# Kernel optimization log

Measured on AMD Instinct MI355X. Metric: run time of the kernel, lower is better.

Reference implementation:

```python
import jax, jax.numpy as jnp
import numpy as np

N_EMBD = 1024
N_HEAD = 16
LN_EPS = 1e-5

def setup_inputs() -> dict:
    key = jax.random.key(0)
    ks = jax.random.split(key, 12)
    B, T, C = 2, 2048, N_EMBD
    s = lambda k, shape, scale=0.02: (jax.random.normal(k, shape, dtype=jnp.float32) * scale)
    return {
        "x": jax.random.normal(ks[0], (B, T, C), dtype=jnp.float32),
        "ln1_g": jnp.ones((C,), jnp.float32),
        "ln1_b": jnp.zeros((C,), jnp.float32),
        "W_attn": s(ks[1], (C, 3 * C)),
        "b_attn": jnp.zeros((3 * C,), jnp.float32),
        "W_o": s(ks[2], (C, C)),
        "b_o": jnp.zeros((C,), jnp.float32),
        "ln2_g": jnp.ones((C,), jnp.float32),
        "ln2_b": jnp.zeros((C,), jnp.float32),
        "W_fc": s(ks[3], (C, 4 * C)),
        "b_fc": jnp.zeros((4 * C,), jnp.float32),
        "W_fc2": s(ks[4], (4 * C, C)),
        "b_fc2": jnp.zeros((C,), jnp.float32),
    }

def _layernorm(x, g, b):
    mu = jnp.mean(x, axis=-1, keepdims=True)
    var = jnp.mean(jnp.square(x - mu), axis=-1, keepdims=True)
    return (x - mu) * jax.lax.rsqrt(var + LN_EPS) * g + b

def reference(x, ln1_g, ln1_b, W_attn, b_attn, W_o, b_o, ln2_g, ln2_b, W_fc, b_fc, W_fc2, b_fc2):
    B, T, C = x.shape
    H, D = N_HEAD, C // N_HEAD
    # ---- attention branch (use_cache=False: T_total == T, causal mask) ----
    h = _layernorm(x, ln1_g, ln1_b)
    qkv = h @ W_attn + b_attn                       # [B,T,3C]
    q, k, v = jnp.split(qkv, 3, axis=-1)
    q = q.reshape(B, T, H, D).transpose(0, 2, 1, 3)  # [B,H,T,D]
    k = k.reshape(B, T, H, D).transpose(0, 2, 1, 3)
    v = v.reshape(B, T, H, D).transpose(0, 2, 1, 3)
    w = jnp.einsum('bhqd,bhkd->bhqk', q, k) / jnp.sqrt(jnp.float32(D))  # [B,H,T,T]
    causal = jnp.tril(jnp.ones((T, T), dtype=bool))
    w = jnp.where(causal, w, jnp.float32(-jnp.inf))
    w = jax.nn.softmax(w, axis=-1)
    y = jnp.einsum('bhqk,bhkd->bhqd', w, v)          # [B,H,T,D]
    y = y.transpose(0, 2, 1, 3).reshape(B, T, C)
    x = x + (y @ W_o + b_o)
    # ---- MLP branch ----
    h2 = _layernorm(x, ln2_g, ln2_b)
    h2 = jax.nn.gelu(h2 @ W_fc + b_fc, approximate=True)  # tanh approx, matches nn.GELU('tanh')
    x = x + (h2 @ W_fc2 + b_fc2)
    return x
```

## Files before the change

kernel.cpp:

```cpp
#include <hip/hip_runtime.h>


typedef unsigned short u16;
typedef unsigned int u32;
typedef __attribute__((ext_vector_type(8))) short v8s;
typedef __attribute__((ext_vector_type(4))) float v4f;

#define GAS __attribute__((address_space(1)))
#define LAS __attribute__((address_space(3)))

__device__ __forceinline__ u16 f2bf(float f) {
  u32 u = __float_as_uint(f);
  u = (u + 0x7FFF + ((u >> 16) & 1)) >> 16;
  return (u16)u;
}
__device__ __forceinline__ u32 f2bf2(float lo, float hi) {
  u32 r;
  asm("v_cvt_pk_bf16_f32 %0, %1, %2" : "=v"(r) : "v"(lo), "v"(hi));
  return r;
}
__device__ __forceinline__ float exp2g(float x) {
  return __builtin_amdgcn_exp2f(x);
}
__device__ __forceinline__ float bf2f(u16 h) {
  return __uint_as_float(((u32)h) << 16);
}
__device__ __forceinline__ float fast_tanh(float x) {
  return 1.f - 2.f / (1.f + __expf(2.f * x));
}

__global__ __launch_bounds__(256)
void wtrans(const float* __restrict__ W, u16* __restrict__ Wt, int K, int N) {
  __shared__ float tile[32][33];
  const int n0 = blockIdx.x << 5, k0 = blockIdx.y << 5;
  const int r = threadIdx.x >> 5, c = threadIdx.x & 31;
#pragma unroll
  for (int i = 0; i < 4; ++i)
    tile[r + 8 * i][c] = W[(size_t)(k0 + r + 8 * i) * N + n0 + c];
  __syncthreads();
#pragma unroll
  for (int i = 0; i < 4; ++i)
    Wt[(size_t)(n0 + r + 8 * i) * K + k0 + c] = f2bf(tile[c][r + 8 * i]);
}

__global__ __launch_bounds__(256)
void ln_bf16(const float* __restrict__ x, const float* __restrict__ g,
             const float* __restrict__ be, u16* __restrict__ out) {
  constexpr int C = 1024;
  const int row = blockIdx.x, t = threadIdx.x;
  const float4 v = ((const float4*)(x + (size_t)row * C))[t];
  float s = v.x + v.y + v.z + v.w;
#pragma unroll
  for (int m = 32; m >= 1; m >>= 1) s += __shfl_xor(s, m);
  __shared__ float red[4], red2[4];
  if ((t & 63) == 0) red[t >> 6] = s;
  __syncthreads();
  const float mu = (red[0] + red[1] + red[2] + red[3]) * (1.f / C);
  const float dx = v.x - mu, dy = v.y - mu, dz = v.z - mu, dw = v.w - mu;
  float s2 = dx * dx + dy * dy + dz * dz + dw * dw;
#pragma unroll
  for (int m = 32; m >= 1; m >>= 1) s2 += __shfl_xor(s2, m);
  if ((t & 63) == 0) red2[t >> 6] = s2;
  __syncthreads();
  const float var = (red2[0] + red2[1] + red2[2] + red2[3]) * (1.f / C);
  const float rs = rsqrtf(var + 1e-5f);
  const int c = t << 2;
  uint2 pk;
  pk.x = f2bf2(dx * rs * g[c + 0] + be[c + 0], dy * rs * g[c + 1] + be[c + 1]);
  pk.y = f2bf2(dz * rs * g[c + 2] + be[c + 2], dw * rs * g[c + 3] + be[c + 3]);
  *(uint2*)(out + (size_t)row * C + c) = pk;
}

template <int EPI>
__global__ __launch_bounds__(512, 2)
void gemm_bt_p256b(const u16* __restrict__ A, const u16* __restrict__ Bt,
                   const float* __restrict__ bias, const float* __restrict__ res,
                   void* __restrict__ outp, int M, int N, int K) {
  __shared__ u16 As[4][256 * 32];
  __shared__ u16 Bs[4][256 * 32];
  const int tid = threadIdx.x;
  const int wave = tid >> 6, lane = tid & 63;
  const int m0 = blockIdx.y << 8, n0 = blockIdx.x << 8;

  v4f acc[8][4];
  const v4f vz = {0.f, 0.f, 0.f, 0.f};
#pragma unroll
  for (int i = 0; i < 8; ++i)
#pragma unroll
    for (int j = 0; j < 4; ++j) acc[i][j] = vz;

  const int wm = (wave >> 2) << 7;
  const int wn = (wave & 3) << 6;
  const int fr = lane & 15;
  const int fg = lane >> 4;

  const int sr = tid >> 2;
  const int sc = (((tid & 3) ^ ((tid >> 4) & 3)) << 3);
  const u16* gA0 = A + (size_t)(m0 + sr) * K + sc;
  const u16* gA1 = gA0 + (size_t)128 * K;
  const u16* gB0 = Bt + (size_t)(n0 + sr) * K + sc;
  const u16* gB1 = gB0 + (size_t)128 * K;
  const int aoff = wave * 512;

  const u32 asb = (u32)(size_t)(LAS const u16*)&As[0][0];
  const u32 bsb = (u32)(size_t)(LAS const u16*)&Bs[0][0];
  const int cgp = fg ^ ((fr >> 2) & 3);
  const u32 afrag = (u32)(((wm + fr) << 6) + (cgp << 4));
  const u32 bfrag = (u32)(((wn + fr) << 6) + (cgp << 4));

  const int nk = K >> 5;

#define PI_A(t, bf)                                                               \
  do {                                                                            \
    const int k0_ = (t) << 5;                                                     \
    __builtin_amdgcn_global_load_lds((GAS const u32*)(gA0 + k0_),                 \
                                     (LAS u32*)(As[bf] + aoff), 16, 0, 0);        \
    __builtin_amdgcn_global_load_lds((GAS const u32*)(gA1 + k0_),                 \
                                     (LAS u32*)(As[bf] + aoff + 4096), 16, 0, 0); \
  } while (0)
#define PI_B(t, bf)                                                               \
  do {                                                                            \
    const int k0_ = (t) << 5;                                                     \
    __builtin_amdgcn_global_load_lds((GAS const u32*)(gB0 + k0_),                 \
                                     (LAS u32*)(Bs[bf] + aoff), 16, 0, 0);        \
    __builtin_amdgcn_global_load_lds((GAS const u32*)(gB1 + k0_),                 \
                                     (LAS u32*)(Bs[bf] + aoff + 4096), 16, 0, 0); \
  } while (0)

  v8s a[8], b[4];
  auto rd0 = [&](int buf) __attribute__((always_inline)) {
    const u32 ab = asb + ((u32)buf << 14) + afrag;
    const u32 bb = bsb + ((u32)buf << 14) + bfrag;
    asm volatile("ds_read_b128 %0, %1 offset:0"    : "=v"(a[0]) : "v"(ab));
    asm volatile("ds_read_b128 %0, %1 offset:1024" : "=v"(a[1]) : "v"(ab));
    asm volatile("ds_read_b128 %0, %1 offset:2048" : "=v"(a[2]) : "v"(ab));
    asm volatile("ds_read_b128 %0, %1 offset:3072" : "=v"(a[3]) : "v"(ab));
    asm volatile("ds_read_b128 %0, %1 offset:0"    : "=v"(b[0]) : "v"(bb));
    asm volatile("ds_read_b128 %0, %1 offset:1024" : "=v"(b[1]) : "v"(bb));
    asm volatile("ds_read_b128 %0, %1 offset:2048" : "=v"(b[2]) : "v"(bb));
    asm volatile("ds_read_b128 %0, %1 offset:3072" : "=v"(b[3]) : "v"(bb));
    asm volatile("s_waitcnt lgkmcnt(0)"
                 : "+v"(a[0]), "+v"(a[1]), "+v"(a[2]), "+v"(a[3]),
                   "+v"(b[0]), "+v"(b[1]), "+v"(b[2]), "+v"(b[3])
                 :
                 : "memory");
  };
  auto rd1 = [&](int buf) __attribute__((always_inline)) {
    const u32 ab = asb + ((u32)buf << 14) + afrag;
    asm volatile("ds_read_b128 %0, %1 offset:4096" : "=v"(a[4]) : "v"(ab));
    asm volatile("ds_read_b128 %0, %1 offset:5120" : "=v"(a[5]) : "v"(ab));
    asm volatile("ds_read_b128 %0, %1 offset:6144" : "=v"(a[6]) : "v"(ab));
    asm volatile("ds_read_b128 %0, %1 offset:7168" : "=v"(a[7]) : "v"(ab));
    asm volatile("s_waitcnt lgkmcnt(0)"
                 : "+v"(a[4]), "+v"(a[5]), "+v"(a[6]), "+v"(a[7])
                 :
                 : "memory");
  };
  auto mfma03 = [&]() __attribute__((always_inline)) {
    __builtin_amdgcn_s_setprio(1);
#pragma unroll
    for (int i = 0; i < 4; ++i)
#pragma unroll
      for (int j = 0; j < 4; ++j)
        acc[i][j] = __builtin_amdgcn_mfma_f32_16x16x32_bf16(a[i], b[j], acc[i][j], 0, 0, 0);
    __builtin_amdgcn_s_setprio(0);
  };
  auto mfma47 = [&]() __attribute__((always_inline)) {
    __builtin_amdgcn_s_setprio(1);
#pragma unroll
    for (int i = 4; i < 8; ++i)
#pragma unroll
      for (int j = 0; j < 4; ++j)
        acc[i][j] = __builtin_amdgcn_mfma_f32_16x16x32_bf16(a[i], b[j], acc[i][j], 0, 0, 0);
    __builtin_amdgcn_s_setprio(0);
  };

  PI_A(0, 0); PI_B(0, 0);
  PI_A(1, 1); PI_B(1, 1);
  PI_A(2, 2); PI_B(2, 2);

  for (int kt = 0; kt < nk - 2; ++kt) {
    asm volatile("s_waitcnt vmcnt(8)" ::: "memory");
    __builtin_amdgcn_s_barrier();
    if (kt + 3 < nk) PI_A(kt + 3, (kt + 3) & 3);
    rd0(kt & 3);
    mfma03();
    __builtin_amdgcn_s_barrier();
    if (kt + 3 < nk) PI_B(kt + 3, (kt + 3) & 3);
    rd1(kt & 3);
    mfma47();
  }
  asm volatile("s_waitcnt vmcnt(4)" ::: "memory");
  __builtin_amdgcn_s_barrier();
  rd0((nk - 2) & 3);
  mfma03();
  __builtin_amdgcn_s_barrier();
  rd1((nk - 2) & 3);
  mfma47();
  asm volatile("s_waitcnt vmcnt(0)" ::: "memory");
  __builtin_amdgcn_s_barrier();
  rd0((nk - 1) & 3);
  mfma03();
  __builtin_amdgcn_s_barrier();
  rd1((nk - 1) & 3);
  mfma47();
#undef PI_A
#undef PI_B

  const int er = (lane >> 4) << 2;
#pragma unroll
  for (int mi = 0; mi < 8; ++mi) {
#pragma unroll
    for (int ni = 0; ni < 4; ++ni) {
      const int col = n0 + wn + ni * 16 + fr;
      const float bcol = bias[col];
#pragma unroll
      for (int r = 0; r < 4; ++r) {
        const int row = m0 + wm + mi * 16 + er + r;
        float v = acc[mi][ni][r] + bcol;
        if constexpr (EPI == 1) {
          const float t = fast_tanh(0.7978845608028654f * (v + 0.044715f * v * v * v));
          v = 0.5f * v * (1.f + t);
        }
        if constexpr (EPI == 2) {
          v += res[(size_t)row * N + col];
          ((float*)outp)[(size_t)row * N + col] = v;
        } else {
          ((u16*)outp)[(size_t)row * N + col] = f2bf(v);
        }
      }
    }
  }
}

template <int EPI, int REMAP>
__global__ __launch_bounds__(256)
void gemm_bt_p(const u16* __restrict__ A, const u16* __restrict__ Bt,
               const float* __restrict__ bias, const float* __restrict__ res,
               void* __restrict__ outp, int M, int N, int K) {
  __shared__ u16 As[3][128 * 32];
  __shared__ u16 Bs[3][128 * 32];
  const int tid = threadIdx.x;
  const int wave = tid >> 6, lane = tid & 63;
  int bx, by;
  if constexpr (REMAP) {
    const int gx = (int)gridDim.x;
    const int wg = blockIdx.y * gx + blockIdx.x;
    const int xcd = wg & 7;
    const int q = wg >> 3;
    bx = q % gx;
    by = xcd + ((q / gx) << 3);
  } else {
    bx = blockIdx.x;
    by = blockIdx.y;
  }
  const int m0 = by << 7, n0 = bx << 7;

  v4f acc[4][4];
  const v4f vz = {0.f, 0.f, 0.f, 0.f};
#pragma unroll
  for (int i = 0; i < 4; ++i)
#pragma unroll
    for (int j = 0; j < 4; ++j) acc[i][j] = vz;

  const int wm = (wave >> 1) << 6, wn = (wave & 1) << 6;
  const int sr = lane >> 2;
  const int sc = (((lane & 3) ^ ((lane >> 4) & 3)) << 3);
  const int fr = lane & 15;
  const int fg = lane >> 4;
  const int c0 = wave << 1;

  const u16* gA0 = A + (size_t)(m0 + c0 * 16 + sr) * K + sc;
  const u16* gA1 = A + (size_t)(m0 + c0 * 16 + 16 + sr) * K + sc;
  const u16* gB0 = Bt + (size_t)(n0 + c0 * 16 + sr) * K + sc;
  const u16* gB1 = Bt + (size_t)(n0 + c0 * 16 + 16 + sr) * K + sc;
  const int aoff = c0 * 512;

  const u32 asb = (u32)(size_t)(LAS const u16*)&As[0][0];
  const u32 bsb = (u32)(size_t)(LAS const u16*)&Bs[0][0];
  const int cgp = fg ^ ((fr >> 2) & 3);
  const u32 afrag = (u32)(((wm + fr) << 6) + (cgp << 4));
  const u32 bfrag = (u32)(((wn + fr) << 6) + (cgp << 4));

  const int nk = K >> 5;

#define P128_ISSUE(t, bf)                                                        \
  do {                                                                           \
    const int k0_ = (t) << 5;                                                    \
    __builtin_amdgcn_global_load_lds((GAS const u32*)(gA0 + k0_),                \
                                     (LAS u32*)(As[bf] + aoff), 16, 0, 0);       \
    __builtin_amdgcn_global_load_lds((GAS const u32*)(gA1 + k0_),                \
                                     (LAS u32*)(As[bf] + aoff + 512), 16, 0, 0); \
    __builtin_amdgcn_global_load_lds((GAS const u32*)(gB0 + k0_),                \
                                     (LAS u32*)(Bs[bf] + aoff), 16, 0, 0);       \
    __builtin_amdgcn_global_load_lds((GAS const u32*)(gB1 + k0_),                \
                                     (LAS u32*)(Bs[bf] + aoff + 512), 16, 0, 0); \
  } while (0)

  auto ldfr = [&](int buf, v8s (&a)[4], v8s (&b)[4]) __attribute__((always_inline)) {
    const u32 ab = asb + ((u32)buf << 13) + afrag;
    const u32 bb = bsb + ((u32)buf << 13) + bfrag;
    asm volatile("ds_read_b128 %0, %1 offset:0"    : "=v"(a[0]) : "v"(ab));
    asm volatile("ds_read_b128 %0, %1 offset:1024" : "=v"(a[1]) : "v"(ab));
    asm volatile("ds_read_b128 %0, %1 offset:2048" : "=v"(a[2]) : "v"(ab));
    asm volatile("ds_read_b128 %0, %1 offset:3072" : "=v"(a[3]) : "v"(ab));
    asm volatile("ds_read_b128 %0, %1 offset:0"    : "=v"(b[0]) : "v"(bb));
    asm volatile("ds_read_b128 %0, %1 offset:1024" : "=v"(b[1]) : "v"(bb));
    asm volatile("ds_read_b128 %0, %1 offset:2048" : "=v"(b[2]) : "v"(bb));
    asm volatile("ds_read_b128 %0, %1 offset:3072" : "=v"(b[3]) : "v"(bb));
  };
  auto wait8 = [&](v8s (&a)[4], v8s (&b)[4]) __attribute__((always_inline)) {
    asm volatile("s_waitcnt lgkmcnt(0)"
                 : "+v"(a[0]), "+v"(a[1]), "+v"(a[2]), "+v"(a[3]),
                   "+v"(b[0]), "+v"(b[1]), "+v"(b[2]), "+v"(b[3])
                 :
                 : "memory");
  };
  auto mfma16 = [&](v8s (&a)[4], v8s (&b)[4]) __attribute__((always_inline)) {
#pragma unroll
    for (int i = 0; i < 4; ++i)
#pragma unroll
      for (int j = 0; j < 4; ++j)
        acc[i][j] = __builtin_amdgcn_mfma_f32_16x16x32_bf16(a[i], b[j], acc[i][j], 0, 0, 0);
  };

  v8s aX[4], bX[4], aY[4], bY[4];

  P128_ISSUE(0, 0);
  P128_ISSUE(1, 1);
  P128_ISSUE(2, 2);
  asm volatile("s_waitcnt vmcnt(8)" ::: "memory");
  __builtin_amdgcn_s_barrier();
  ldfr(0, aX, bX);
  wait8(aX, bX);

  int br = 1, bi = 0;
  for (int kt = 0; kt < nk - 2; kt += 2) {
    asm volatile("s_waitcnt vmcnt(4)" ::: "memory");
    __builtin_amdgcn_s_barrier();
    ldfr(br, aY, bY);
    if (kt + 3 < nk) P128_ISSUE(kt + 3, bi);
    __builtin_amdgcn_sched_barrier(0);
    mfma16(aX, bX);
    wait8(aY, bY);
    br = (br == 2) ? 0 : br + 1;
    bi = (bi == 2) ? 0 : bi + 1;
    asm volatile("s_waitcnt vmcnt(4)" ::: "memory");
    __builtin_amdgcn_s_barrier();
    ldfr(br, aX, bX);
    if (kt + 4 < nk) P128_ISSUE(kt + 4, bi);
    __builtin_amdgcn_sched_barrier(0);
    mfma16(aY, bY);
    wait8(aX, bX);
    br = (br == 2) ? 0 : br + 1;
    bi = (bi == 2) ? 0 : bi + 1;
  }
  asm volatile("s_waitcnt vmcnt(0)" ::: "memory");
  __builtin_amdgcn_s_barrier();
  ldfr(br, aY, bY);
  __builtin_amdgcn_sched_barrier(0);
  mfma16(aX, bX);
  wait8(aY, bY);
  mfma16(aY, bY);
#undef P128_ISSUE

  const int er = (lane >> 4) << 2;
#pragma unroll
  for (int mi = 0; mi < 4; ++mi) {
#pragma unroll
    for (int ni = 0; ni < 4; ++ni) {
      const int col = n0 + wn + ni * 16 + fr;
      const float bcol = bias[col];
#pragma unroll
      for (int r = 0; r < 4; ++r) {
        const int row = m0 + wm + mi * 16 + er + r;
        float v = acc[mi][ni][r] + bcol;
        if constexpr (EPI == 1) {
          const float t = fast_tanh(0.7978845608028654f * (v + 0.044715f * v * v * v));
          v = 0.5f * v * (1.f + t);
        }
        if constexpr (EPI == 2) {
          v += res[(size_t)row * N + col];
          ((float*)outp)[(size_t)row * N + col] = v;
        } else {
          ((u16*)outp)[(size_t)row * N + col] = f2bf(v);
        }
      }
    }
  }
}

template <int EPI>
__global__ __launch_bounds__(256)
void gemm_bt_n64(const u16* __restrict__ A, const u16* __restrict__ Bt,
                 const float* __restrict__ bias, const float* __restrict__ res,
                 void* __restrict__ outp, int M, int N, int K) {
  __shared__ u16 As[4][128 * 32];
  __shared__ u16 Bs[4][64 * 32];
  const int tid = threadIdx.x;
  const int wave = tid >> 6, lane = tid & 63;
  const int m0 = blockIdx.y << 7, n0 = blockIdx.x << 6;

  v4f acc[4][2];
  const v4f vz = {0.f, 0.f, 0.f, 0.f};
#pragma unroll
  for (int i = 0; i < 4; ++i)
#pragma unroll
    for (int j = 0; j < 2; ++j) acc[i][j] = vz;

  const int wm = (wave >> 1) << 6, wn = (wave & 1) << 5;
  const int sr = lane >> 2;
  const int sc = (((lane & 3) ^ ((lane >> 4) & 3)) << 3);
  const int fr = lane & 15;
  const int fg = lane >> 4;

  const u16* gA0 = A + (size_t)(m0 + wave * 32 + sr) * K + sc;
  const u16* gA1 = A + (size_t)(m0 + wave * 32 + 16 + sr) * K + sc;
  const u16* gB0 = Bt + (size_t)(n0 + wave * 16 + sr) * K + sc;
  const int aoff = wave * 1024;
  const int boff = wave * 512;

  const u32 asb = (u32)(size_t)(LAS const u16*)&As[0][0];
  const u32 bsb = (u32)(size_t)(LAS const u16*)&Bs[0][0];
  const int cgp = fg ^ ((fr >> 2) & 3);
  const u32 afrag = (u32)(((wm + fr) << 6) + (cgp << 4));
  const u32 bfrag = (u32)(((wn + fr) << 6) + (cgp << 4));

  const int nk = K >> 5;

#define N64_ISSUE(t, bf)                                                      \
  do {                                                                        \
    const int k0_ = (t) << 5;                                                 \
    __builtin_amdgcn_global_load_lds((GAS const u32*)(gA0 + k0_),             \
                                     (LAS u32*)(As[bf] + aoff), 16, 0, 0);    \
    __builtin_amdgcn_global_load_lds((GAS const u32*)(gA1 + k0_),             \
                                     (LAS u32*)(As[bf] + aoff + 512), 16, 0, 0); \
    __builtin_amdgcn_global_load_lds((GAS const u32*)(gB0 + k0_),             \
                                     (LAS u32*)(Bs[bf] + boff), 16, 0, 0);    \
  } while (0)

  N64_ISSUE(0, 0);
  N64_ISSUE(1, 1);
  N64_ISSUE(2, 2);

  auto compute = [&](int kt) __attribute__((always_inline)) {
    const u32 ab = asb + ((u32)(kt & 3) << 13) + afrag;
    const u32 bb = bsb + ((u32)(kt & 3) << 12) + bfrag;
    v8s a0, a1, a2, a3, b0, b1;
    asm volatile("ds_read_b128 %0, %1 offset:0"    : "=v"(a0) : "v"(ab));
    asm volatile("ds_read_b128 %0, %1 offset:1024" : "=v"(a1) : "v"(ab));
    asm volatile("ds_read_b128 %0, %1 offset:2048" : "=v"(a2) : "v"(ab));
    asm volatile("ds_read_b128 %0, %1 offset:3072" : "=v"(a3) : "v"(ab));
    asm volatile("ds_read_b128 %0, %1 offset:0"    : "=v"(b0) : "v"(bb));
    asm volatile("ds_read_b128 %0, %1 offset:1024" : "=v"(b1) : "v"(bb));
    asm volatile("s_waitcnt lgkmcnt(0)"
                 : "+v"(a0), "+v"(a1), "+v"(a2), "+v"(a3), "+v"(b0), "+v"(b1)
                 :
                 : "memory");
    acc[0][0] = __builtin_amdgcn_mfma_f32_16x16x32_bf16(a0, b0, acc[0][0], 0, 0, 0);
    acc[0][1] = __builtin_amdgcn_mfma_f32_16x16x32_bf16(a0, b1, acc[0][1], 0, 0, 0);
    acc[1][0] = __builtin_amdgcn_mfma_f32_16x16x32_bf16(a1, b0, acc[1][0], 0, 0, 0);
    acc[1][1] = __builtin_amdgcn_mfma_f32_16x16x32_bf16(a1, b1, acc[1][1], 0, 0, 0);
    acc[2][0] = __builtin_amdgcn_mfma_f32_16x16x32_bf16(a2, b0, acc[2][0], 0, 0, 0);
    acc[2][1] = __builtin_amdgcn_mfma_f32_16x16x32_bf16(a2, b1, acc[2][1], 0, 0, 0);
    acc[3][0] = __builtin_amdgcn_mfma_f32_16x16x32_bf16(a3, b0, acc[3][0], 0, 0, 0);
    acc[3][1] = __builtin_amdgcn_mfma_f32_16x16x32_bf16(a3, b1, acc[3][1], 0, 0, 0);
  };

  for (int kt = 0; kt < nk - 2; ++kt) {
    asm volatile("s_waitcnt vmcnt(6)" ::: "memory");
    __builtin_amdgcn_s_barrier();
    if (kt + 3 < nk) N64_ISSUE(kt + 3, (kt + 3) & 3);
    compute(kt);
  }
  asm volatile("s_waitcnt vmcnt(3)" ::: "memory");
  __builtin_amdgcn_s_barrier();
  compute(nk - 2);
  asm volatile("s_waitcnt vmcnt(0)" ::: "memory");
  __builtin_amdgcn_s_barrier();
  compute(nk - 1);
#undef N64_ISSUE

  const int er = (lane >> 4) << 2;
#pragma unroll
  for (int mi = 0; mi < 4; ++mi) {
#pragma unroll
    for (int ni = 0; ni < 2; ++ni) {
      const int col = n0 + wn + ni * 16 + fr;
      const float bcol = bias[col];
#pragma unroll
      for (int r = 0; r < 4; ++r) {
        const int row = m0 + wm + mi * 16 + er + r;
        float v = acc[mi][ni][r] + bcol;
        if constexpr (EPI == 1) {
          const float t = fast_tanh(0.7978845608028654f * (v + 0.044715f * v * v * v));
          v = 0.5f * v * (1.f + t);
        }
        if constexpr (EPI == 2) {
          v += res[(size_t)row * N + col];
          ((float*)outp)[(size_t)row * N + col] = v;
        } else {
          ((u16*)outp)[(size_t)row * N + col] = f2bf(v);
        }
      }
    }
  }
}

__global__ __launch_bounds__(256)
void transpose_v(const u16* __restrict__ qkv, u16* __restrict__ Vt) {
  __shared__ u16 tile[64][65];
  const int t0 = blockIdx.x << 6;
  const int bh = blockIdx.y;
  const int b = bh >> 4, h = bh & 15;
  const int r4 = threadIdx.x >> 6, c = threadIdx.x & 63;
#pragma unroll
  for (int i = 0; i < 16; ++i) {
    const int r = r4 * 16 + i;
    tile[r][c] = qkv[(size_t)(b * 2048 + t0 + r) * 3072 + 2048 + h * 64 + c];
  }
  __syncthreads();
#pragma unroll
  for (int i = 0; i < 16; ++i) {
    const int d = r4 * 16 + i;
    Vt[(size_t)bh * 64 * 2048 + (size_t)d * 2048 + t0 + c] = tile[c][d];
  }
}

constexpr int PSTR = 72;
constexpr float ATT_SC = 0.18033688011112042f;

template <bool MASKED>
__device__ __forceinline__ void soft16(
    const v4f (&st)[4], float (&e)[4][4], v4f (&ot)[4],
    float& m_i, float& l_i, const int kb, const int qrow,
    const int fr, const int fg) {
  const int q = qrow + fr;
#pragma unroll
  for (int ks = 0; ks < 4; ++ks) {
    const v4f sv = st[ks] * ATT_SC;
#pragma unroll
    for (int r = 0; r < 4; ++r) {
      float v = sv[r];
      if (MASKED) v = (kb + ks * 16 + fg * 4 + r <= q) ? v : -1e30f;
      e[ks][r] = v;
    }
  }
  float mk0 = fmaxf(fmaxf(e[0][0], e[0][1]), fmaxf(e[0][2], e[0][3]));
  float mk1 = fmaxf(fmaxf(e[1][0], e[1][1]), fmaxf(e[1][2], e[1][3]));
  float mk2 = fmaxf(fmaxf(e[2][0], e[2][1]), fmaxf(e[2][2], e[2][3]));
  float mk3 = fmaxf(fmaxf(e[3][0], e[3][1]), fmaxf(e[3][2], e[3][3]));
  float mt = fmaxf(fmaxf(mk0, mk1), fmaxf(mk2, mk3));
  mt = fmaxf(mt, __shfl_xor(mt, 16));
  mt = fmaxf(mt, __shfl_xor(mt, 32));
  if (__any(mt > m_i)) {
    const float m_new = fmaxf(m_i, mt);
    const float alpha = exp2g(m_i - m_new);
    m_i = m_new;
    l_i *= alpha;
#pragma unroll
    for (int ds = 0; ds < 4; ++ds) ot[ds] *= alpha;
  }
#pragma unroll
  for (int ks = 0; ks < 4; ++ks)
#pragma unroll
    for (int r = 0; r < 4; ++r) e[ks][r] = exp2g(e[ks][r] - m_i);
  float s0 = (e[0][0] + e[0][1]) + (e[0][2] + e[0][3]);
  float s1 = (e[1][0] + e[1][1]) + (e[1][2] + e[1][3]);
  float s2 = (e[2][0] + e[2][1]) + (e[2][2] + e[2][3]);
  float s3 = (e[3][0] + e[3][1]) + (e[3][2] + e[3][3]);
  float ls = (s0 + s1) + (s2 + s3);
  ls += __shfl_xor(ls, 16);
  ls += __shfl_xor(ls, 32);
  l_i += ls;
}

__device__ __forceinline__ void pstore(const float (&e)[4][4],
                                       u16* __restrict__ pw,
                                       const int fr, const int fg) {
#pragma unroll
  for (int ks = 0; ks < 4; ++ks) {
    uint2 pk;
    pk.x = f2bf2(e[ks][0], e[ks][1]);
    pk.y = f2bf2(e[ks][2], e[ks][3]);
    *(uint2*)&pw[fr * PSTR + ks * 16 + fg * 4] = pk;
  }
}

__device__ __forceinline__ void pvacc(const v8s (&vfr)[4][2],
                                      const u16* __restrict__ pw,
                                      v4f (&ot)[4], const int fr, const int fg) {
  const v8s pf0 = *(const v8s*)&pw[fr * PSTR + fg * 8];
  const v8s pf1 = *(const v8s*)&pw[fr * PSTR + 32 + fg * 8];
  __builtin_amdgcn_s_setprio(1);
#pragma unroll
  for (int ds = 0; ds < 4; ++ds) {
    ot[ds] = __builtin_amdgcn_mfma_f32_16x16x32_bf16(vfr[ds][0], pf0, ot[ds], 0, 0, 0);
    ot[ds] = __builtin_amdgcn_mfma_f32_16x16x32_bf16(vfr[ds][1], pf1, ot[ds], 0, 0, 0);
  }
  __builtin_amdgcn_s_setprio(0);
}

template <bool MASKED>
__device__ __forceinline__ void attn_sub(
    const v8s (&kf)[4][2], const v8s (&vfr)[4][2], const v8s (&qf)[2],
    v4f (&ot)[4], float& m_i, float& l_i, u16* __restrict__ pw,
    const int kb, const int qrow, const int fr, const int fg) {
  const v4f vz = {0.f, 0.f, 0.f, 0.f};
  v4f st[4];
  __builtin_amdgcn_s_setprio(1);
#pragma unroll
  for (int ks = 0; ks < 4; ++ks) {
    st[ks] = vz;
    st[ks] = __builtin_amdgcn_mfma_f32_16x16x32_bf16(kf[ks][0], qf[0], st[ks], 0, 0, 0);
    st[ks] = __builtin_amdgcn_mfma_f32_16x16x32_bf16(kf[ks][1], qf[1], st[ks], 0, 0, 0);
  }
  __builtin_amdgcn_s_setprio(0);
  float e[4][4];
  soft16<MASKED>(st, e, ot, m_i, l_i, kb, qrow, fr, fg);
  pstore(e, pw, fr, fg);
  pvacc(vfr, pw, ot, fr, fg);
}

template <bool MASKA>
__device__ __forceinline__ void attn_sub_pair(
    const v8s (&kf)[4][2], const v8s (&vfr)[4][2],
    const v8s (&qfA)[2], const v8s (&qfB)[2],
    v4f (&otA)[4], v4f (&otB)[4],
    float& mA, float& lA, float& mB, float& lB,
    u16* __restrict__ pwA, u16* __restrict__ pwB,
    const int kb, const int rowA, const int rowB, const int fr, const int fg) {
  const v4f vz = {0.f, 0.f, 0.f, 0.f};
  v4f stA[4], stB[4];
  __builtin_amdgcn_s_setprio(1);
#pragma unroll
  for (int ks = 0; ks < 4; ++ks) {
    stA[ks] = vz;
    stA[ks] = __builtin_amdgcn_mfma_f32_16x16x32_bf16(kf[ks][0], qfA[0], stA[ks], 0, 0, 0);
    stA[ks] = __builtin_amdgcn_mfma_f32_16x16x32_bf16(kf[ks][1], qfA[1], stA[ks], 0, 0, 0);
  }
#pragma unroll
  for (int ks = 0; ks < 4; ++ks) {
    stB[ks] = vz;
    stB[ks] = __builtin_amdgcn_mfma_f32_16x16x32_bf16(kf[ks][0], qfB[0], stB[ks], 0, 0, 0);
    stB[ks] = __builtin_amdgcn_mfma_f32_16x16x32_bf16(kf[ks][1], qfB[1], stB[ks], 0, 0, 0);
  }
  __builtin_amdgcn_s_setprio(0);
  float eA[4][4];
  soft16<MASKA>(stA, eA, otA, mA, lA, kb, rowA, fr, fg);
  pstore(eA, pwA, fr, fg);
  float eB[4][4];
  soft16<false>(stB, eB, otB, mB, lB, kb, rowB, fr, fg);
  pvacc(vfr, pwA, otA, fr, fg);
  pstore(eB, pwB, fr, fg);
  pvacc(vfr, pwB, otB, fr, fg);
}

__global__ __launch_bounds__(256)
void attn_kernel(const u16* __restrict__ qkv, const u16* __restrict__ Vt,
                 u16* __restrict__ y) {
  constexpr int T = 2048, D = 64, C = 1024, QS = 3072;
  __shared__ alignas(16) u16 Ktile[2][64 * 64];
  __shared__ alignas(16) u16 Vtile[2][64 * 64];
  __shared__ alignas(16) u16 Pw[8][16 * PSTR];

  const int tid = threadIdx.x, wave = tid >> 6, lane = tid & 63;
  const int fr = lane & 15, fg = lane >> 4;
  const int wg = blockIdx.y * 16 + blockIdx.x;
  const int xcd = wg & 7, seq = wg >> 3;
  const int bh = ((seq & 3) << 3) + xcd;
  const int ta = seq >> 2, tb = 31 - ta;
  const int b = bh >> 4, h = bh & 15;
  const u16* qkvb = qkv + (size_t)b * T * QS + h * 64;
  const u16* Kg = qkvb + 1024;
  const u16* Vh = Vt + (size_t)bh * D * T;
  u16* pwA = &Pw[wave][0];
  u16* pwB = &Pw[4 + wave][0];

  const int rowA = ta * 64 + wave * 16;
  const int rowB = tb * 64 + wave * 16;

  v8s qfA[2], qfB[2];
#pragma unroll
  for (int dh = 0; dh < 2; ++dh) {
    qfA[dh] = *(const v8s*)&qkvb[(size_t)(rowA + fr) * QS + dh * 32 + fg * 8];
    qfB[dh] = *(const v8s*)&qkvb[(size_t)(rowB + fr) * QS + dh * 32 + fg * 8];
  }

  const v4f vz = {0.f, 0.f, 0.f, 0.f};
  v4f otA[4], otB[4];
#pragma unroll
  for (int ds = 0; ds < 4; ++ds) { otA[ds] = vz; otB[ds] = vz; }
  float mA = -1e30f, lA = 0.f, mB = -1e30f, lB = 0.f;

  const int srow = lane >> 3;
  const int sg0 = lane & 7;

  const int nt = tb + 1;
  {
#pragma unroll
    for (int cc = 0; cc < 2; ++cc) {
      const int r0 = wave * 16 + cc * 8;
      const int rr = r0 + srow;
      const int gg = sg0 ^ (rr & 7);
      __builtin_amdgcn_global_load_lds(
          (GAS const u32*)(Kg + (size_t)rr * QS + gg * 8),
          (LAS u32*)(Ktile[0] + r0 * 64), 16, 0, 0);
      __builtin_amdgcn_global_load_lds(
          (GAS const u32*)(Vh + (size_t)rr * T + gg * 8),
          (LAS u32*)(Vtile[0] + r0 * 64), 16, 0, 0);
    }
  }
  for (int kt = 0; kt < nt; ++kt) {
    __syncthreads();
    if (kt + 1 < nt) {
      const int kb1 = (kt + 1) << 6;
      const int nb = (kt + 1) & 1;
#pragma unroll
      for (int cc = 0; cc < 2; ++cc) {
        const int r0 = wave * 16 + cc * 8;
        const int rr = r0 + srow;
        const int gg = sg0 ^ (rr & 7);
        __builtin_amdgcn_global_load_lds(
            (GAS const u32*)(Kg + (size_t)(kb1 + rr) * QS + gg * 8),
            (LAS u32*)(Ktile[nb] + r0 * 64), 16, 0, 0);
        __builtin_amdgcn_global_load_lds(
            (GAS const u32*)(Vh + (size_t)rr * T + kb1 + gg * 8),
            (LAS u32*)(Vtile[nb] + r0 * 64), 16, 0, 0);
      }
    }
    const u16* Kt = Ktile[kt & 1];
    const u16* Vi = Vtile[kt & 1];
    const int kb = kt << 6;
    const int swz = fr & 7;
    v8s kf[4][2], vfr[4][2];
#pragma unroll
    for (int ks = 0; ks < 4; ++ks) {
      const int rr = ks * 16 + fr;
      kf[ks][0] = *(const v8s*)&Kt[rr * 64 + ((0 + fg) ^ swz) * 8];
      kf[ks][1] = *(const v8s*)&Kt[rr * 64 + ((4 + fg) ^ swz) * 8];
      vfr[ks][0] = *(const v8s*)&Vi[rr * 64 + ((0 + fg) ^ swz) * 8];
      vfr[ks][1] = *(const v8s*)&Vi[rr * 64 + ((4 + fg) ^ swz) * 8];
    }
    if (kt < ta) {
      attn_sub_pair<false>(kf, vfr, qfA, qfB, otA, otB, mA, lA, mB, lB,
                           pwA, pwB, kb, rowA, rowB, fr, fg);
    } else if (kt == ta) {
      attn_sub_pair<true>(kf, vfr, qfA, qfB, otA, otB, mA, lA, mB, lB,
                          pwA, pwB, kb, rowA, rowB, fr, fg);
    } else if (kt < tb) {
      attn_sub<false>(kf, vfr, qfB, otB, mB, lB, pwB, kb, rowB, fr, fg);
    } else {
      attn_sub<true>(kf, vfr, qfB, otB, mB, lB, pwB, kb, rowB, fr, fg);
    }
  }

  const float invA = 1.f / lA, invB = 1.f / lB;
#pragma unroll
  for (int ds = 0; ds < 4; ++ds) {
    uint2 pa, pb;
    pa.x = f2bf2(otA[ds][0] * invA, otA[ds][1] * invA);
    pa.y = f2bf2(otA[ds][2] * invA, otA[ds][3] * invA);
    pb.x = f2bf2(otB[ds][0] * invB, otB[ds][1] * invB);
    pb.y = f2bf2(otB[ds][2] * invB, otB[ds][3] * invB);
    *(uint2*)&y[(size_t)(b * T + rowA + fr) * C + h * D + ds * 16 + fg * 4] = pa;
    *(uint2*)&y[(size_t)(b * T + rowB + fr) * C + h * D + ds * 16 + fg * 4] = pb;
  }
}

extern "C" void kernel_launch(void* const* d_in, const int* in_sizes, int n_in,
                              void* d_out, int out_size, void* d_ws, size_t ws_size,
                              hipStream_t stream) {
  const float* x      = (const float*)d_in[0];
  const float* ln1_g  = (const float*)d_in[1];
  const float* ln1_b  = (const float*)d_in[2];
  const float* W_attn = (const float*)d_in[3];
  const float* b_attn = (const float*)d_in[4];
  const float* W_o    = (const float*)d_in[5];
  const float* b_o    = (const float*)d_in[6];
  const float* ln2_g  = (const float*)d_in[7];
  const float* ln2_b  = (const float*)d_in[8];
  const float* W_fc   = (const float*)d_in[9];
  const float* b_fc   = (const float*)d_in[10];
  const float* W_fc2  = (const float*)d_in[11];
  const float* b_fc2  = (const float*)d_in[12];
  float* out = (float*)d_out;
  char* ws = (char*)d_ws;

  const size_t MB = 1u << 20;
  u16* Wattn_t = (u16*)(ws + 0 * MB);
  u16* Wo_t    = (u16*)(ws + 6 * MB);
  u16* Wfc_t   = (u16*)(ws + 8 * MB);
  u16* Wfc2_t  = (u16*)(ws + 16 * MB);
  float* x1    = (float*)(ws + 24 * MB);
  u16* h1      = (u16*)(ws + 40 * MB);
  u16* qkv     = (u16*)(ws + 48 * MB);
  u16* Vt      = (u16*)(ws + 88 * MB);
  u16* yb      = (u16*)(ws + 40 * MB);
  u16* h2      = (u16*)(ws + 48 * MB);
  u16* ab      = (u16*)(ws + 56 * MB);

  wtrans<<<dim3(3072 / 32, 1024 / 32), 256, 0, stream>>>(W_attn, Wattn_t, 1024, 3072);
  wtrans<<<dim3(1024 / 32, 1024 / 32), 256, 0, stream>>>(W_o, Wo_t, 1024, 1024);
  wtrans<<<dim3(4096 / 32, 1024 / 32), 256, 0, stream>>>(W_fc, Wfc_t, 1024, 4096);
  wtrans<<<dim3(1024 / 32, 4096 / 32), 256, 0, stream>>>(W_fc2, Wfc2_t, 4096, 1024);

  ln_bf16<<<4096, 256, 0, stream>>>(x, ln1_g, ln1_b, h1);
  gemm_bt_p<0, 0><<<dim3(3072 / 128, 4096 / 128), 256, 0, stream>>>(
      h1, Wattn_t, b_attn, nullptr, qkv, 4096, 3072, 1024);
  transpose_v<<<dim3(2048 / 64, 32), 256, 0, stream>>>(qkv, Vt);
  attn_kernel<<<dim3(16, 32), 256, 0, stream>>>(qkv, Vt, yb);
  gemm_bt_n64<2><<<dim3(1024 / 64, 4096 / 128), 256, 0, stream>>>(
      yb, Wo_t, b_o, x, x1, 4096, 1024, 1024);
  ln_bf16<<<4096, 256, 0, stream>>>(x1, ln2_g, ln2_b, h2);
  gemm_bt_p256b<1><<<dim3(4096 / 256, 4096 / 256), 512, 0, stream>>>(
      h2, Wfc_t, b_fc, nullptr, ab, 4096, 4096, 1024);
  gemm_bt_p<2, 1><<<dim3(1024 / 128, 4096 / 128), 256, 0, stream>>>(
      ab, Wfc2_t, b_fc2, x1, out, 4096, 1024, 4096);
}
```

Measured before the change: 339.5 us.

## Use 8-wave 4-stage pipelined GEMM kernel for FC2 projection

Adds a new 128x128 tile GEMM variant with 512 threads (8 waves, each computing a 64x32 sub-tile) and a 4-buffer LDS ring that keeps three k-tiles in flight via direct global-to-LDS loads. It replaces the 256-thread 3-buffer kernel for the FC2 GEMM (K=4096). The aim is more waves per block to hide latency and a deeper prefetch pipeline over the long K loop. In exchange each wave does fewer MFMAs per barrier, so synchronisation overhead per unit of work grows, and LDS use per block rises to 64 KB.

```diff
diff --git a/kernel.cpp b/kernel.cpp
--- a/kernel.cpp
+++ b/kernel.cpp
@@ -234,6 +234,137 @@
 }
 
 template <int EPI, int REMAP>
+__global__ __launch_bounds__(512, 2)
+void gemm_bt_p128w8(const u16* __restrict__ A, const u16* __restrict__ Bt,
+                    const float* __restrict__ bias, const float* __restrict__ res,
+                    void* __restrict__ outp, int M, int N, int K) {
+  __shared__ u16 As[4][128 * 32];
+  __shared__ u16 Bs[4][128 * 32];
+  const int tid = threadIdx.x;
+  const int wave = tid >> 6, lane = tid & 63;
+  int bx, by;
+  if constexpr (REMAP) {
+    const int gx = (int)gridDim.x;
+    const int wg = blockIdx.y * gx + blockIdx.x;
+    const int xcd = wg & 7;
+    const int q = wg >> 3;
+    bx = q % gx;
+    by = xcd + ((q / gx) << 3);
+  } else {
+    bx = blockIdx.x;
+    by = blockIdx.y;
+  }
+  const int m0 = by << 7, n0 = bx << 7;
+
+  v4f acc[4][2];
+  const v4f vz = {0.f, 0.f, 0.f, 0.f};
+#pragma unroll
+  for (int i = 0; i < 4; ++i)
+#pragma unroll
+    for (int j = 0; j < 2; ++j) acc[i][j] = vz;
+
+  const int wm = (wave >> 2) << 6;
+  const int wn = (wave & 3) << 5;
+  const int fr = lane & 15;
+  const int fg = lane >> 4;
+
+  const int sr = tid >> 2;
+  const int sc = (((tid & 3) ^ ((tid >> 4) & 3)) << 3);
+  const u16* gA0 = A + (size_t)(m0 + sr) * K + sc;
+  const u16* gB0 = Bt + (size_t)(n0 + sr) * K + sc;
+  const int aoff = wave * 512;
+
+  const u32 asb = (u32)(size_t)(LAS const u16*)&As[0][0];
+  const u32 bsb = (u32)(size_t)(LAS const u16*)&Bs[0][0];
+  const int cgp = fg ^ ((fr >> 2) & 3);
+  const u32 afrag = (u32)(((wm + fr) << 6) + (cgp << 4));
+  const u32 bfrag = (u32)(((wn + fr) << 6) + (cgp << 4));
+
+  const int nk = K >> 5;
+
+#define W8_ISSUE(t, bf)                                                       \
+  do {                                                                        \
+    const int k0_ = (t) << 5;                                                 \
+    __builtin_amdgcn_global_load_lds((GAS const u32*)(gA0 + k0_),             \
+                                     (LAS u32*)(As[bf] + aoff), 16, 0, 0);    \
+    __builtin_amdgcn_global_load_lds((GAS const u32*)(gB0 + k0_),             \
+                                     (LAS u32*)(Bs[bf] + aoff), 16, 0, 0);    \
+  } while (0)
+
+  auto step = [&](int buf) __attribute__((always_inline)) {
+    const u32 ab = asb + ((u32)buf << 13) + afrag;
+    const u32 bb = bsb + ((u32)buf << 13) + bfrag;
+    v8s a0, a1, a2, a3, b0, b1;
+    asm volatile("ds_read_b128 %0, %1 offset:0"    : "=v"(a0) : "v"(ab));
+    asm volatile("ds_read_b128 %0, %1 offset:1024" : "=v"(a1) : "v"(ab));
+    asm volatile("ds_read_b128 %0, %1 offset:2048" : "=v"(a2) : "v"(ab));
+    asm volatile("ds_read_b128 %0, %1 offset:3072" : "=v"(a3) : "v"(ab));
+    asm volatile("ds_read_b128 %0, %1 offset:0"    : "=v"(b0) : "v"(bb));
+    asm volatile("ds_read_b128 %0, %1 offset:1024" : "=v"(b1) : "v"(bb));
+    asm volatile("s_waitcnt lgkmcnt(0)"
+                 : "+v"(a0), "+v"(a1), "+v"(a2), "+v"(a3), "+v"(b0), "+v"(b1)
+                 :
+                 : "memory");
+    __builtin_amdgcn_s_setprio(1);
+    acc[0][0] = __builtin_amdgcn_mfma_f32_16x16x32_bf16(a0, b0, acc[0][0], 0, 0, 0);
+    acc[0][1] = __builtin_amdgcn_mfma_f32_16x16x32_bf16(a0, b1, acc[0][1], 0, 0, 0);
+    acc[1][0] = __builtin_amdgcn_mfma_f32_16x16x32_bf16(a1, b0, acc[1][0], 0, 0, 0);
+    acc[1][1] = __builtin_amdgcn_mfma_f32_16x16x32_bf16(a1, b1, acc[1][1], 0, 0, 0);
+    acc[2][0] = __builtin_amdgcn_mfma_f32_16x16x32_bf16(a2, b0, acc[2][0], 0, 0, 0);
+    acc[2][1] = __builtin_amdgcn_mfma_f32_16x16x32_bf16(a2, b1, acc[2][1], 0, 0, 0);
+    acc[3][0] = __builtin_amdgcn_mfma_f32_16x16x32_bf16(a3, b0, acc[3][0], 0, 0, 0);
+    acc[3][1] = __builtin_amdgcn_mfma_f32_16x16x32_bf16(a3, b1, acc[3][1], 0, 0, 0);
+    __builtin_amdgcn_s_setprio(0);
+  };
+
+  W8_ISSUE(0, 0);
+  W8_ISSUE(1, 1);
+  W8_ISSUE(2, 2);
+
+  for (int kt = 0; kt < nk - 3; ++kt) {
+    asm volatile("s_waitcnt vmcnt(4)" ::: "memory");
+    __builtin_amdgcn_s_barrier();
+    W8_ISSUE(kt + 3, (kt + 3) & 3);
+    step(kt & 3);
+  }
+  asm volatile("s_waitcnt vmcnt(4)" ::: "memory");
+  __builtin_amdgcn_s_barrier();
+  step((nk - 3) & 3);
+  asm volatile("s_waitcnt vmcnt(2)" ::: "memory");
+  __builtin_amdgcn_s_barrier();
+  step((nk - 2) & 3);
+  asm volatile("s_waitcnt vmcnt(0)" ::: "memory");
+  __builtin_amdgcn_s_barrier();
+  step((nk - 1) & 3);
+#undef W8_ISSUE
+
+  const int er = (lane >> 4) << 2;
+#pragma unroll
+  for (int mi = 0; mi < 4; ++mi) {
+#pragma unroll
+    for (int ni = 0; ni < 2; ++ni) {
+      const int col = n0 + wn + ni * 16 + fr;
+      const float bcol = bias[col];
+#pragma unroll
+      for (int r = 0; r < 4; ++r) {
+        const int row = m0 + wm + mi * 16 + er + r;
+        float v = acc[mi][ni][r] + bcol;
+        if constexpr (EPI == 1) {
+          const float t = fast_tanh(0.7978845608028654f * (v + 0.044715f * v * v * v));
+          v = 0.5f * v * (1.f + t);
+        }
+        if constexpr (EPI == 2) {
+          v += res[(size_t)row * N + col];
+          ((float*)outp)[(size_t)row * N + col] = v;
+        } else {
+          ((u16*)outp)[(size_t)row * N + col] = f2bf(v);
+        }
+      }
+    }
+  }
+}
+
+template <int EPI, int REMAP>
 __global__ __launch_bounds__(256)
 void gemm_bt_p(const u16* __restrict__ A, const u16* __restrict__ Bt,
                const float* __restrict__ bias, const float* __restrict__ res,
@@ -815,6 +946,6 @@
   ln_bf16<<<4096, 256, 0, stream>>>(x1, ln2_g, ln2_b, h2);
   gemm_bt_p256b<1><<<dim3(4096 / 256, 4096 / 256), 512, 0, stream>>>(
       h2, Wfc_t, b_fc, nullptr, ab, 4096, 4096, 1024);
-  gemm_bt_p<2, 1><<<dim3(1024 / 128, 4096 / 128), 256, 0, stream>>>(
+  gemm_bt_p128w8<2, 1><<<dim3(1024 / 128, 4096 / 128), 512, 0, stream>>>(
       ab, Wfc2_t, b_fc2, x1, out, 4096, 1024, 4096);
 }
```

New measurement: 338.8 us. About the same (-0.2%).
